# Kernel optimization log

Measured on AMD Instinct MI355X. Metric: run time of the kernel, lower is better.

## Reference

```python
import jax, jax.numpy as jnp
import numpy as np

IOU_THRESHOLD = 0.5

def cxcywh_to_xyxy(b):
    cx, cy, w, h = jnp.split(b, 4, axis=-1)
    return jnp.concatenate([cx - 0.5 * w, cy - 0.5 * h, cx + 0.5 * w, cy + 0.5 * h], axis=-1)

def batched_giou(p_xyxy, t_xyxy):
    # p_xyxy: [B, N, 4], t_xyxy: [B, T, 4] -> giou: [B, N, T]
    p = p_xyxy[:, :, None, :]  # [B, N, 1, 4]
    t = t_xyxy[:, None, :, :]  # [B, 1, T, 4]
    area_p = (p_xyxy[..., 2] - p_xyxy[..., 0]) * (p_xyxy[..., 3] - p_xyxy[..., 1])  # [B, N]
    area_t = (t_xyxy[..., 2] - t_xyxy[..., 0]) * (t_xyxy[..., 3] - t_xyxy[..., 1])  # [B, T]
    lt = jnp.maximum(p[..., :2], t[..., :2])
    rb = jnp.minimum(p[..., 2:], t[..., 2:])
    wh = jnp.clip(rb - lt, 0.0)
    inter = wh[..., 0] * wh[..., 1]  # [B, N, T]
    union = area_p[:, :, None] + area_t[:, None, :] - inter
    iou = inter / union
    # enclosing box
    lt_e = jnp.minimum(p[..., :2], t[..., :2])
    rb_e = jnp.maximum(p[..., 2:], t[..., 2:])
    wh_e = jnp.clip(rb_e - lt_e, 0.0)
    area_e = wh_e[..., 0] * wh_e[..., 1]
    return iou - (area_e - union) / area_e

def setup_inputs() -> dict:
    key = jax.random.key(0)
    k1, k2 = jax.random.split(key)
    B, N, T = 128, 900, 300
    pred_boxes = jax.random.uniform(k1, (B, N, 4), dtype=jnp.float32)
    target_boxes = jax.random.uniform(k2, (B, T, 4), dtype=jnp.float32)
    target_mask = jnp.ones((B, T), dtype=bool)
    return {"pred_boxes": pred_boxes, "target_boxes": target_boxes, "target_mask": target_mask}

def reference(pred_boxes, target_boxes, target_mask):
    # pred_boxes: [B, N, 4] cxcywh; target_boxes: [B, T, 4] cxcywh (padded)
    p_xyxy = cxcywh_to_xyxy(pred_boxes)
    t_xyxy = cxcywh_to_xyxy(target_boxes)
    giou = batched_giou(p_xyxy, t_xyxy)  # [B, N, T]
    max_iou = jnp.max(giou, axis=1)      # [B, T] best GIoU per target
    pred_idx = jnp.argmax(giou, axis=1)  # [B, T] matched query per target
    valid = target_mask & (max_iou >= IOU_THRESHOLD)  # [B, T] match kept
    return pred_idx, valid, max_iou
```

## Files before the change

### kernel.cpp

```cpp
#include <hip/hip_runtime.h>


#define BB 128
#define NN 900
#define TT 300
#define TCHUNK 64
#define NGROUPS 4
#define NSLICE 225
#define TBLOCKS 5

__global__ __launch_bounds__(256) void simple_matcher_kernel(
    const float* __restrict__ pred,
    const float* __restrict__ tgt,
    const unsigned char* __restrict__ mask,
    float* __restrict__ out)
{
#pragma clang fp contract(off)
    __shared__ float spx0[NN], spy0[NN], spx1[NN], spy1[NN], spa[NN];
    __shared__ float sbest[256];
    __shared__ int   sbidx[256];

    const int b   = blockIdx.x / TBLOCKS;
    const int tc  = blockIdx.x % TBLOCKS;
    const int tid = threadIdx.x;
    const int tl  = tid & 63;
    const int ng  = tid >> 6;
    const int t   = tc * TCHUNK + tl;

    for (int i = tid; i < NN; i += 256) {
        const float4 pb = ((const float4*)pred)[b * NN + i];
        float x0 = pb.x - 0.5f * pb.z;
        float y0 = pb.y - 0.5f * pb.w;
        float x1 = pb.x + 0.5f * pb.z;
        float y1 = pb.y + 0.5f * pb.w;
        spx0[i] = x0; spy0[i] = y0; spx1[i] = x1; spy1[i] = y1;
        spa[i]  = (x1 - x0) * (y1 - y0);
    }
    __syncthreads();

    float tx0 = 0.f, ty0 = 0.f, tx1 = 0.f, ty1 = 0.f, ta = 0.f;
    if (t < TT) {
        const float4 tb = ((const float4*)tgt)[b * TT + t];
        tx0 = tb.x - 0.5f * tb.z;
        ty0 = tb.y - 0.5f * tb.w;
        tx1 = tb.x + 0.5f * tb.z;
        ty1 = tb.y + 0.5f * tb.w;
        ta  = (tx1 - tx0) * (ty1 - ty0);
    }

    float best = -INFINITY;
    int   bidx = 0;
    const int n0 = ng * NSLICE;
    for (int k = 0; k < NSLICE; ++k) {
        const int n = n0 + k;
        const float px0 = spx0[n], py0 = spy0[n];
        const float px1 = spx1[n], py1 = spy1[n];
        const float pa  = spa[n];

        const float ltx = fmaxf(px0, tx0);
        const float lty = fmaxf(py0, ty0);
        const float rbx = fminf(px1, tx1);
        const float rby = fminf(py1, ty1);
        const float w   = fmaxf(rbx - ltx, 0.f);
        const float h   = fmaxf(rby - lty, 0.f);
        const float inter = w * h;
        const float uni   = pa + ta - inter;
        const float iou   = inter / uni;

        const float ex0 = fminf(px0, tx0);
        const float ey0 = fminf(py0, ty0);
        const float ex1 = fmaxf(px1, tx1);
        const float ey1 = fmaxf(py1, ty1);
        const float ew  = fmaxf(ex1 - ex0, 0.f);
        const float eh  = fmaxf(ey1 - ey0, 0.f);
        const float ea  = ew * eh;
        const float g   = iou - (ea - uni) / ea;

        if (g > best) { best = g; bidx = n; }
    }

    sbest[tid] = best;
    sbidx[tid] = bidx;
    __syncthreads();

    if (ng == 0 && t < TT) {
        for (int s = 1; s < NGROUPS; ++s) {
            const float v = sbest[s * 64 + tl];
            const int   i = sbidx[s * 64 + tl];
            if (v > best) { best = v; bidx = i; }
        }
        const int bt = b * TT + t;
        const bool valid = (mask[bt] != 0) && (best >= 0.5f);
        out[bt]              = (float)bidx;
        out[BB * TT + bt]    = valid ? 1.f : 0.f;
        out[2 * BB * TT + bt] = best;
    }
}

extern "C" void kernel_launch(void* const* d_in, const int* in_sizes, int n_in,
                              void* d_out, int out_size, void* d_ws, size_t ws_size,
                              hipStream_t stream) {
    const float* pred = (const float*)d_in[0];
    const float* tgt  = (const float*)d_in[1];
    const unsigned char* mask = (const unsigned char*)d_in[2];
    float* out = (float*)d_out;

    dim3 grid(BB * TBLOCKS);
    dim3 block(256);
    simple_matcher_kernel<<<grid, block, 0, stream>>>(pred, tgt, mask, out);
}
```

Measured before the change: 116.9 us.

## Split prediction scan across blocks and add a second reduction kernel

Splits the 900 predictions into 5 slices, one per block, raising the grid from 640 to 3200 blocks. Each block stores its partial best GIoU and index to workspace, and a new reduce kernel merges the slices and writes the outputs. Predictions are now held in shared memory as one float4 per box, with the area recomputed in the inner loop. This targets low occupancy and a long serial loop per thread, at the cost of a second launch, extra global traffic, and the first-max tie rule now depending on slice order.

```diff
diff --git a/kernel.cpp b/kernel.cpp
--- a/kernel.cpp
+++ b/kernel.cpp
@@ -5,36 +5,37 @@
 #define NN 900
 #define TT 300
 #define TCHUNK 64
-#define NGROUPS 4
-#define NSLICE 225
 #define TBLOCKS 5
+#define NSPLIT 5
+#define NPB 180
+#define NPW 45
 
-__global__ __launch_bounds__(256) void simple_matcher_kernel(
+__global__ __launch_bounds__(256) void matcher_scan_kernel(
     const float* __restrict__ pred,
     const float* __restrict__ tgt,
-    const unsigned char* __restrict__ mask,
-    float* __restrict__ out)
+    float2* __restrict__ part)
 {
 #pragma clang fp contract(off)
-    __shared__ float spx0[NN], spy0[NN], spx1[NN], spy1[NN], spa[NN];
-    __shared__ float sbest[256];
-    __shared__ int   sbidx[256];
+    __shared__ float4 sp[NPB];
+    __shared__ float  sbest[256];
+    __shared__ int    sbidx[256];
 
-    const int b   = blockIdx.x / TBLOCKS;
-    const int tc  = blockIdx.x % TBLOCKS;
+    const int ns  = blockIdx.x % NSPLIT;
+    const int tc  = (blockIdx.x / NSPLIT) % TBLOCKS;
+    const int b   = blockIdx.x / (NSPLIT * TBLOCKS);
     const int tid = threadIdx.x;
     const int tl  = tid & 63;
     const int ng  = tid >> 6;
     const int t   = tc * TCHUNK + tl;
 
-    for (int i = tid; i < NN; i += 256) {
-        const float4 pb = ((const float4*)pred)[b * NN + i];
-        float x0 = pb.x - 0.5f * pb.z;
-        float y0 = pb.y - 0.5f * pb.w;
-        float x1 = pb.x + 0.5f * pb.z;
-        float y1 = pb.y + 0.5f * pb.w;
-        spx0[i] = x0; spy0[i] = y0; spx1[i] = x1; spy1[i] = y1;
-        spa[i]  = (x1 - x0) * (y1 - y0);
+    if (tid < NPB) {
+        const float4 pb = ((const float4*)pred)[b * NN + ns * NPB + tid];
+        float4 q;
+        q.x = pb.x - 0.5f * pb.z;
+        q.y = pb.y - 0.5f * pb.w;
+        q.z = pb.x + 0.5f * pb.z;
+        q.w = pb.y + 0.5f * pb.w;
+        sp[tid] = q;
     }
     __syncthreads();
 
@@ -50,33 +51,23 @@
 
     float best = -INFINITY;
     int   bidx = 0;
-    const int n0 = ng * NSLICE;
-    for (int k = 0; k < NSLICE; ++k) {
-        const int n = n0 + k;
-        const float px0 = spx0[n], py0 = spy0[n];
-        const float px1 = spx1[n], py1 = spy1[n];
-        const float pa  = spa[n];
+    const int k0 = ng * NPW;
+    for (int k = 0; k < NPW; ++k) {
+        const float4 p = sp[k0 + k];
+        const float pa = (p.z - p.x) * (p.w - p.y);
 
-        const float ltx = fmaxf(px0, tx0);
-        const float lty = fmaxf(py0, ty0);
-        const float rbx = fminf(px1, tx1);
-        const float rby = fminf(py1, ty1);
-        const float w   = fmaxf(rbx - ltx, 0.f);
-        const float h   = fmaxf(rby - lty, 0.f);
+        const float w   = fmaxf(fminf(p.z, tx1) - fmaxf(p.x, tx0), 0.f);
+        const float h   = fmaxf(fminf(p.w, ty1) - fmaxf(p.y, ty0), 0.f);
         const float inter = w * h;
         const float uni   = pa + ta - inter;
         const float iou   = inter / uni;
 
-        const float ex0 = fminf(px0, tx0);
-        const float ey0 = fminf(py0, ty0);
-        const float ex1 = fmaxf(px1, tx1);
-        const float ey1 = fmaxf(py1, ty1);
-        const float ew  = fmaxf(ex1 - ex0, 0.f);
-        const float eh  = fmaxf(ey1 - ey0, 0.f);
+        const float ew  = fmaxf(fmaxf(p.z, tx1) - fminf(p.x, tx0), 0.f);
+        const float eh  = fmaxf(fmaxf(p.w, ty1) - fminf(p.y, ty0), 0.f);
         const float ea  = ew * eh;
         const float g   = iou - (ea - uni) / ea;
 
-        if (g > best) { best = g; bidx = n; }
+        if (g > best) { best = g; bidx = k0 + k; }
     }
 
     sbest[tid] = best;
@@ -84,17 +75,36 @@
     __syncthreads();
 
     if (ng == 0 && t < TT) {
-        for (int s = 1; s < NGROUPS; ++s) {
+        for (int s = 1; s < 4; ++s) {
             const float v = sbest[s * 64 + tl];
             const int   i = sbidx[s * 64 + tl];
             if (v > best) { best = v; bidx = i; }
         }
-        const int bt = b * TT + t;
-        const bool valid = (mask[bt] != 0) && (best >= 0.5f);
-        out[bt]              = (float)bidx;
-        out[BB * TT + bt]    = valid ? 1.f : 0.f;
-        out[2 * BB * TT + bt] = best;
+        float2 pr;
+        pr.x = best;
+        pr.y = __int_as_float(ns * NPB + bidx);
+        part[(b * TT + t) * NSPLIT + ns] = pr;
     }
+}
+
+__global__ __launch_bounds__(256) void matcher_reduce_kernel(
+    const float2* __restrict__ part,
+    const unsigned char* __restrict__ mask,
+    float* __restrict__ out)
+{
+    const int bt = blockIdx.x * 256 + threadIdx.x;
+    if (bt >= BB * TT) return;
+
+    float best = -INFINITY;
+    int   bidx = 0;
+    for (int s = 0; s < NSPLIT; ++s) {
+        const float2 pr = part[bt * NSPLIT + s];
+        if (pr.x > best) { best = pr.x; bidx = __float_as_int(pr.y); }
+    }
+    const bool valid = (mask[bt] != 0) && (best >= 0.5f);
+    out[bt]               = (float)bidx;
+    out[BB * TT + bt]     = valid ? 1.f : 0.f;
+    out[2 * BB * TT + bt] = best;
 }
 
 extern "C" void kernel_launch(void* const* d_in, const int* in_sizes, int n_in,
@@ -104,8 +114,10 @@
     const float* tgt  = (const float*)d_in[1];
     const unsigned char* mask = (const unsigned char*)d_in[2];
     float* out = (float*)d_out;
+    float2* part = (float2*)d_ws;
 
-    dim3 grid(BB * TBLOCKS);
-    dim3 block(256);
-    simple_matcher_kernel<<<grid, block, 0, stream>>>(pred, tgt, mask, out);
+    matcher_scan_kernel<<<dim3(BB * TBLOCKS * NSPLIT), dim3(256), 0, stream>>>(
+        pred, tgt, part);
+    matcher_reduce_kernel<<<dim3((BB * TT + 255) / 256), dim3(256), 0, stream>>>(
+        part, mask, out);
 }
```

New measurement: 111.0 us. 5.0% less time.

## Use approximate fast GIoU scan with top-2 margin check and exact fallback

Applied to the files above, without the earlier changes.

Replaces the two-divide GIoU in the inner loop with one algebraically combined numerator times a hardware reciprocal. It also tracks the second-best score per target, stores predictions as packed float4 in shared memory, and splits the query range across 8 waves with 512 threads. The winning candidate is recomputed exactly. Targets whose top-two margin falls below a threshold get a full exact rescan by a whole wave, which keeps argmax and max bit-faithful. The risk is extra fallback work if many near-ties occur, plus higher register and shared-memory pressure.

```diff
diff --git a/kernel.cpp b/kernel.cpp
--- a/kernel.cpp
+++ b/kernel.cpp
@@ -5,95 +5,157 @@
 #define NN 900
 #define TT 300
 #define TCHUNK 64
-#define NGROUPS 4
-#define NSLICE 225
 #define TBLOCKS 5
+#define NWAVES 8
+#define MARGIN 2e-5f
 
-__global__ __launch_bounds__(256) void simple_matcher_kernel(
+__device__ __forceinline__ float giou_exact(float4 pb, float4 tb) {
+#pragma clang fp contract(off)
+    float px0 = pb.x - 0.5f * pb.z, py0 = pb.y - 0.5f * pb.w;
+    float px1 = pb.x + 0.5f * pb.z, py1 = pb.y + 0.5f * pb.w;
+    float tx0 = tb.x - 0.5f * tb.z, ty0 = tb.y - 0.5f * tb.w;
+    float tx1 = tb.x + 0.5f * tb.z, ty1 = tb.y + 0.5f * tb.w;
+    float pa = (px1 - px0) * (py1 - py0);
+    float ta = (tx1 - tx0) * (ty1 - ty0);
+    float w  = fmaxf(fminf(px1, tx1) - fmaxf(px0, tx0), 0.f);
+    float h  = fmaxf(fminf(py1, ty1) - fmaxf(py0, ty0), 0.f);
+    float inter = w * h;
+    float uni   = pa + ta - inter;
+    float iou   = inter / uni;
+    float ew = fmaxf(fmaxf(px1, tx1) - fminf(px0, tx0), 0.f);
+    float eh = fmaxf(fmaxf(py1, ty1) - fminf(py0, ty0), 0.f);
+    float ea = ew * eh;
+    return iou - (ea - uni) / ea;
+}
+
+__global__ __launch_bounds__(512) void matcher_kernel(
     const float* __restrict__ pred,
     const float* __restrict__ tgt,
     const unsigned char* __restrict__ mask,
     float* __restrict__ out)
 {
-#pragma clang fp contract(off)
-    __shared__ float spx0[NN], spy0[NN], spx1[NN], spy1[NN], spa[NN];
-    __shared__ float sbest[256];
-    __shared__ int   sbidx[256];
+    __shared__ float4 sp[NN];
+    __shared__ float  rbv[NWAVES * TCHUNK], rsv[NWAVES * TCHUNK];
+    __shared__ int    riv[NWAVES * TCHUNK];
+    __shared__ int    sflag[TCHUNK];
+    __shared__ int    scount;
 
+    const int tc  = blockIdx.x % TBLOCKS;
     const int b   = blockIdx.x / TBLOCKS;
-    const int tc  = blockIdx.x % TBLOCKS;
     const int tid = threadIdx.x;
-    const int tl  = tid & 63;
-    const int ng  = tid >> 6;
-    const int t   = tc * TCHUNK + tl;
+    const int l   = tid & 63;
+    const int wv  = tid >> 6;
+    const int t   = tc * TCHUNK + l;
 
-    for (int i = tid; i < NN; i += 256) {
+    if (tid == 0) scount = 0;
+
+    for (int i = tid; i < NN; i += 512) {
         const float4 pb = ((const float4*)pred)[b * NN + i];
-        float x0 = pb.x - 0.5f * pb.z;
-        float y0 = pb.y - 0.5f * pb.w;
-        float x1 = pb.x + 0.5f * pb.z;
-        float y1 = pb.y + 0.5f * pb.w;
-        spx0[i] = x0; spy0[i] = y0; spx1[i] = x1; spy1[i] = y1;
-        spa[i]  = (x1 - x0) * (y1 - y0);
+        float4 q;
+        q.x = pb.x - 0.5f * pb.z;
+        q.y = pb.y - 0.5f * pb.w;
+        q.z = pb.x + 0.5f * pb.z;
+        q.w = pb.y + 0.5f * pb.w;
+        sp[i] = q;
     }
-    __syncthreads();
 
-    float tx0 = 0.f, ty0 = 0.f, tx1 = 0.f, ty1 = 0.f, ta = 0.f;
+    float tx0 = 0.f, ty0 = 0.f, tx1 = 0.f, ty1 = 0.f, ta = 0.f, wtx = 0.f, wty = 0.f;
     if (t < TT) {
         const float4 tb = ((const float4*)tgt)[b * TT + t];
         tx0 = tb.x - 0.5f * tb.z;
         ty0 = tb.y - 0.5f * tb.w;
         tx1 = tb.x + 0.5f * tb.z;
         ty1 = tb.y + 0.5f * tb.w;
-        ta  = (tx1 - tx0) * (ty1 - ty0);
+        wtx = tx1 - tx0;
+        wty = ty1 - ty0;
+        ta  = wtx * wty;
+    }
+    __syncthreads();
+
+    const int start = wv * 112 + min(wv, 4);
+    const int len   = 112 + (wv < 4 ? 1 : 0);
+
+    float best = -INFINITY, sec = -INFINITY;
+    int   bidxl = 0;
+    #pragma unroll 4
+    for (int k = 0; k < len; ++k) {
+        const float4 q = sp[start + k];
+        const float wpx = q.z - q.x;
+        const float wpy = q.w - q.y;
+        const float pa  = wpx * wpy;
+
+        const float ew = fmaxf(q.z, tx1) - fminf(q.x, tx0);
+        const float eh = fmaxf(q.w, ty1) - fminf(q.y, ty0);
+        const float w  = fmaxf((wpx + wtx) - ew, 0.f);
+        const float h  = fmaxf((wpy + wty) - eh, 0.f);
+        const float inter = w * h;
+        const float ea    = ew * eh;
+        const float uni   = (pa + ta) - inter;
+        const float den   = uni * ea;
+        const float num = fmaf(inter, ea, fmaf(uni, uni, -den));
+        const float g   = num * __builtin_amdgcn_rcpf(den);
+
+        sec = __builtin_amdgcn_fmed3f(g, best, sec);
+        if (g > best) bidxl = k;
+        best = fmaxf(best, g);
     }
 
-    float best = -INFINITY;
-    int   bidx = 0;
-    const int n0 = ng * NSLICE;
-    for (int k = 0; k < NSLICE; ++k) {
-        const int n = n0 + k;
-        const float px0 = spx0[n], py0 = spy0[n];
-        const float px1 = spx1[n], py1 = spy1[n];
-        const float pa  = spa[n];
-
-        const float ltx = fmaxf(px0, tx0);
-        const float lty = fmaxf(py0, ty0);
-        const float rbx = fminf(px1, tx1);
-        const float rby = fminf(py1, ty1);
-        const float w   = fmaxf(rbx - ltx, 0.f);
-        const float h   = fmaxf(rby - lty, 0.f);
-        const float inter = w * h;
-        const float uni   = pa + ta - inter;
-        const float iou   = inter / uni;
-
-        const float ex0 = fminf(px0, tx0);
-        const float ey0 = fminf(py0, ty0);
-        const float ex1 = fmaxf(px1, tx1);
-        const float ey1 = fmaxf(py1, ty1);
-        const float ew  = fmaxf(ex1 - ex0, 0.f);
-        const float eh  = fmaxf(ey1 - ey0, 0.f);
-        const float ea  = ew * eh;
-        const float g   = iou - (ea - uni) / ea;
-
-        if (g > best) { best = g; bidx = n; }
-    }
-
-    sbest[tid] = best;
-    sbidx[tid] = bidx;
+    rbv[wv * TCHUNK + l] = best;
+    rsv[wv * TCHUNK + l] = sec;
+    riv[wv * TCHUNK + l] = start + bidxl;
     __syncthreads();
 
-    if (ng == 0 && t < TT) {
-        for (int s = 1; s < NGROUPS; ++s) {
-            const float v = sbest[s * 64 + tl];
-            const int   i = sbidx[s * 64 + tl];
-            if (v > best) { best = v; bidx = i; }
+    if (tid < TCHUNK && t < TT) {
+        float bb = -INFINITY, ss = -INFINITY;
+        int   bi = 0;
+        #pragma unroll
+        for (int s = 0; s < NWAVES; ++s) {
+            const float ob = rbv[s * TCHUNK + tid];
+            const float os = rsv[s * TCHUNK + tid];
+            const int   oi = riv[s * TCHUNK + tid];
+            ss = fmaxf(fminf(bb, ob), fmaxf(ss, os));
+            if (ob > bb) { bb = ob; bi = oi; }
         }
         const int bt = b * TT + t;
-        const bool valid = (mask[bt] != 0) && (best >= 0.5f);
-        out[bt]              = (float)bidx;
-        out[BB * TT + bt]    = valid ? 1.f : 0.f;
-        out[2 * BB * TT + bt] = best;
+        if (bb - ss > MARGIN) {
+            const float4 pb = ((const float4*)pred)[b * NN + bi];
+            const float4 tb = ((const float4*)tgt)[bt];
+            const float g = giou_exact(pb, tb);
+            const bool valid = (mask[bt] != 0) && (g >= 0.5f);
+            out[bt]               = (float)bi;
+            out[BB * TT + bt]     = valid ? 1.f : 0.f;
+            out[2 * BB * TT + bt] = g;
+        } else {
+            const int pos = atomicAdd(&scount, 1);
+            sflag[pos] = t;
+        }
+    }
+    __syncthreads();
+
+    const int cnt = scount;
+    for (int f = wv; f < cnt; f += NWAVES) {
+        const int ft  = sflag[f];
+        const int fbt = b * TT + ft;
+        const float4 tb = ((const float4*)tgt)[fbt];
+
+        float bx = -INFINITY;
+        int   bi = NN;
+        for (int n = l; n < NN; n += 64) {
+            const float4 pb = ((const float4*)pred)[b * NN + n];
+            const float g = giou_exact(pb, tb);
+            if (g > bx) { bx = g; bi = n; }
+        }
+        for (int off = 32; off >= 1; off >>= 1) {
+            const float ob = __shfl_xor(bx, off);
+            const int   oi = __shfl_xor(bi, off);
+            if (ob > bx || (ob == bx && oi < bi)) { bx = ob; bi = oi; }
+        }
+        if (l == 0) {
+            const bool valid = (mask[fbt] != 0) && (bx >= 0.5f);
+            out[fbt]               = (float)bi;
+            out[BB * TT + fbt]     = valid ? 1.f : 0.f;
+            out[2 * BB * TT + fbt] = bx;
+        }
     }
 }
 
@@ -105,7 +167,6 @@
     const unsigned char* mask = (const unsigned char*)d_in[2];
     float* out = (float*)d_out;
 
-    dim3 grid(BB * TBLOCKS);
-    dim3 block(256);
-    simple_matcher_kernel<<<grid, block, 0, stream>>>(pred, tgt, mask, out);
+    matcher_kernel<<<dim3(BB * TBLOCKS), dim3(512), 0, stream>>>(
+        pred, tgt, mask, out);
 }
```

Measured after the change: 95.61 us. 1.22x faster.
